# Optimization experiments

Hardware: AMD Instinct MI355X
Metric: run time of the kernel (lower is better)

Reference implementation:

```python
import jax, jax.numpy as jnp
import numpy as np

B, L, D, H = 4, 2048, 1024, 16
DH = D // H

def setup_inputs() -> dict:
    key = jax.random.key(0)
    ks = jax.random.split(key, 9)
    s = 1.0 / np.sqrt(D)
    x = jax.random.normal(ks[0], (B, L, D), dtype=jnp.float32)
    Wq = jax.random.uniform(ks[1], (D, D), jnp.float32, -s, s)
    bq = jax.random.uniform(ks[2], (D,), jnp.float32, -s, s)
    Wk = jax.random.uniform(ks[3], (D, D), jnp.float32, -s, s)
    bk = jax.random.uniform(ks[4], (D,), jnp.float32, -s, s)
    Wv = jax.random.uniform(ks[5], (D, D), jnp.float32, -s, s)
    bv = jax.random.uniform(ks[6], (D,), jnp.float32, -s, s)
    Wo = jax.random.uniform(ks[7], (D, D), jnp.float32, -s, s)
    bo = jax.random.uniform(ks[8], (D,), jnp.float32, -s, s)
    mask = jnp.tril(jnp.ones((L, L), dtype=jnp.int32))[None, None]  # [1,1,L,L] causal
    return {"x": x, "Wq": Wq, "bq": bq, "Wk": Wk, "bk": bk, "Wv": Wv, "bv": bv,
            "Wo": Wo, "bo": bo, "mask": mask}

def reference(x, Wq, bq, Wk, bk, Wv, bv, Wo, bo, mask):
    # projections (torch Linear: x @ W.T + b; here W stored transposed already as [D,D])
    q = (x @ Wq + bq).reshape(B, L, H, DH).transpose(0, 2, 1, 3)  # [B,H,L,Dh]
    k = (x @ Wk + bk).reshape(B, L, H, DH).transpose(0, 2, 1, 3)
    v = (x @ Wv + bv).reshape(B, L, H, DH).transpose(0, 2, 1, 3)
    scores = jnp.einsum('bhqd,bhkd->bhqk', q, k) / jnp.sqrt(jnp.float32(DH))
    scores = jnp.where(mask == 0, -jnp.inf, scores)
    attn = jax.nn.softmax(scores, axis=-1)
    out = jnp.einsum('bhqk,bhkd->bhqd', attn, v)  # [B,H,L,Dh]
    out = out.transpose(0, 2, 1, 3).reshape(B, L, D)
    return out @ Wo + bo
```

## Files before the change

### kernel.cpp

```cpp
#include <hip/hip_runtime.h>
#include <hip/hip_bf16.h>


typedef __bf16 bf16;
typedef __bf16 bf16x4 __attribute__((ext_vector_type(4)));
typedef __bf16 bf16x8 __attribute__((ext_vector_type(8)));
typedef float f32x4 __attribute__((ext_vector_type(4)));

#define DEV static __device__ __forceinline__

constexpr int B = 4, L = 2048, D = 1024, H = 16, DH = 64;
constexpr int BL = B * L;
constexpr int GM = 8192, GK = 1024;
constexpr int BKg = 64;
constexpr int PST = 72;

typedef __attribute__((address_space(1))) const void* gptr1;
typedef __attribute__((address_space(3))) void* lptr3;

DEV void load_lds16(const bf16* g, bf16* l) {
  __builtin_amdgcn_global_load_lds((gptr1)g, (lptr3)l, 16, 0, 0);
}

DEV f32x4 mfma(bf16x8 a, bf16x8 b, f32x4 c) {
  return __builtin_amdgcn_mfma_f32_16x16x32_bf16(a, b, c, 0, 0, 0);
}

DEV float scrub(float v) { return (v == v) ? v : 0.f; }

__global__ void sniff_k(const unsigned short* __restrict__ xr, int* flag) {
  __shared__ int cnt;
  if (threadIdx.x == 0) cnt = 0;
  __syncthreads();
  int local = 0;
  for (int i = threadIdx.x; i < 4096; i += 64) {
    const unsigned short u = xr[2 * i];
    const int e = (u >> 7) & 0xFF;
    if (e >= 0x70 && e <= 0x85) local++;
  }
  atomicAdd(&cnt, local);
  __syncthreads();
  if (threadIdx.x == 0) *flag = (cnt > 2048) ? 1 : 0;
}

__global__ __launch_bounds__(256) void cvt_x_k(const void* __restrict__ src,
                                               bf16* __restrict__ dst,
                                               const int* __restrict__ flag, int n) {
  const bool isbf = (*flag != 0);
  const int stride = gridDim.x * blockDim.x * 8;
  for (int idx = (blockIdx.x * blockDim.x + threadIdx.x) * 8; idx < n; idx += stride) {
    bf16x8 o;
    if (isbf) {
      bf16x8 v = *(const bf16x8*)((const bf16*)src + idx);
      #pragma unroll
      for (int j = 0; j < 8; ++j) o[j] = (bf16)scrub((float)v[j]);
    } else {
      const float* s = (const float*)src + idx;
      #pragma unroll
      for (int j = 0; j < 8; ++j) o[j] = (bf16)scrub(s[j]);
    }
    *(bf16x8*)&dst[idx] = o;
  }
}

__global__ __launch_bounds__(256) void wtrans_cvt4_k(const void* __restrict__ W0,
                                                     const void* __restrict__ W1,
                                                     const void* __restrict__ W2,
                                                     const void* __restrict__ W3,
                                                     bf16* __restrict__ dstBase,
                                                     const int* __restrict__ flag) {
  __shared__ bf16 t[32][33];
  const bool isbf = (*flag != 0);
  const int z = blockIdx.z;
  const void* src = (z == 0) ? W0 : (z == 1) ? W1 : (z == 2) ? W2 : W3;
  bf16* dst = dstBase + (size_t)z * D * D;
  const int bx = blockIdx.x * 32, by = blockIdx.y * 32;
  const int tx = threadIdx.x & 31, ty = threadIdx.x >> 5;
  for (int i = ty; i < 32; i += 8) {
    const size_t off = (size_t)(by + i) * D + bx + tx;
    const float v = isbf ? (float)((const bf16*)src)[off] : ((const float*)src)[off];
    t[i][tx] = (bf16)scrub(v);
  }
  __syncthreads();
  for (int i = ty; i < 32; i += 8)
    dst[(size_t)(bx + i) * D + by + tx] = t[tx][i];
}

__global__ __launch_bounds__(256) void vtrans_k(const bf16* __restrict__ V,
                                                bf16* __restrict__ VT) {
  __shared__ __align__(16) bf16 t[64 * 72];
  const int l0 = blockIdx.x * 64, bh = blockIdx.y;
  const int b = bh >> 4, h = bh & 15;
  const int tid = threadIdx.x;
  #pragma unroll
  for (int i = 0; i < 2; ++i) {
    const int o = tid * 8 + i * 2048;
    const int lrow = o >> 6, dcol = o & 63;
    *(bf16x8*)&t[lrow * 72 + dcol] =
        *(const bf16x8*)&V[(size_t)(b * L + l0 + lrow) * D + h * 64 + dcol];
  }
  __syncthreads();
  const int d = tid >> 2, lg = (tid & 3) * 16;
  bf16x8 o0, o1;
  #pragma unroll
  for (int j = 0; j < 8; ++j) o0[j] = t[(lg + j) * 72 + d];
  #pragma unroll
  for (int j = 0; j < 8; ++j) o1[j] = t[(lg + 8 + j) * 72 + d];
  bf16* dst = VT + ((size_t)bh * DH + d) * L + l0 + lg;
  *(bf16x8*)dst = o0;
  *(bf16x8*)(dst + 8) = o1;
}

__global__ __launch_bounds__(256) void qkv_gemm_k(const bf16* __restrict__ A,
                                                  const bf16* __restrict__ Bt,
                                                  const void* __restrict__ bq,
                                                  const void* __restrict__ bk,
                                                  const void* __restrict__ bv,
                                                  bf16* __restrict__ Q,
                                                  bf16* __restrict__ Kk,
                                                  bf16* __restrict__ V,
                                                  const int* __restrict__ flag) {
  __shared__ __align__(16) bf16 As[128 * BKg];
  __shared__ __align__(16) bf16 Bs[128 * BKg];
  const bool isbf = (*flag != 0);
  const int m0 = blockIdx.x * 128, n0 = blockIdx.y * 128;
  const int buf = n0 >> 10, nloc = n0 & 1023;
  bf16* Cb = (buf == 0) ? Q : (buf == 1) ? Kk : V;
  const void* bias = (buf == 0) ? bq : (buf == 1) ? bk : bv;
  const float scale = (buf == 0) ? 0.18033688011111f : 1.0f;

  const int tid = threadIdx.x, wave = tid >> 6, lane = tid & 63;
  const int wr = wave >> 1, wc = wave & 1;
  const int quad = lane >> 4, l16 = lane & 15;
  const int srow = lane >> 3;
  const int scol = ((lane ^ srow) & 7) * 8;
  const int l7 = l16 & 7;
  const int s0 = ((quad ^ l7) * 8);
  const int s1 = s0 ^ 32;

  f32x4 acc[4][4] = {};

  for (int k0 = 0; k0 < GK; k0 += BKg) {
    for (int c = wave; c < 16; c += 4) {
      load_lds16(A  + (size_t)(m0 + c * 8 + srow) * GK + k0 + scol, &As[c * 512]);
      load_lds16(Bt + (size_t)(n0 + c * 8 + srow) * GK + k0 + scol, &Bs[c * 512]);
    }
    __syncthreads();
    #pragma unroll
    for (int kk = 0; kk < BKg; kk += 32) {
      const int sk = kk ? s1 : s0;
      bf16x8 af[4], bfr[4];
      #pragma unroll
      for (int i = 0; i < 4; ++i)
        af[i] = *(const bf16x8*)&As[(wr * 64 + i * 16 + l16) * BKg + sk];
      #pragma unroll
      for (int i = 0; i < 4; ++i)
        bfr[i] = *(const bf16x8*)&Bs[(wc * 64 + i * 16 + l16) * BKg + sk];
      #pragma unroll
      for (int mi = 0; mi < 4; ++mi)
        #pragma unroll
        for (int ni = 0; ni < 4; ++ni)
          acc[mi][ni] = mfma(af[mi], bfr[ni], acc[mi][ni]);
    }
    __syncthreads();
  }

  #pragma unroll
  for (int ni = 0; ni < 4; ++ni) {
    const int col = nloc + wc * 64 + ni * 16 + l16;
    const float bv2 = isbf ? (float)((const bf16*)bias)[col] : ((const float*)bias)[col];
    #pragma unroll
    for (int mi = 0; mi < 4; ++mi)
      #pragma unroll
      for (int r = 0; r < 4; ++r) {
        const int row = m0 + wr * 64 + mi * 16 + quad * 4 + r;
        Cb[(size_t)row * D + col] = (bf16)((acc[mi][ni][r] + bv2) * scale);
      }
  }
}

__global__ __launch_bounds__(256) void gemm_bt_k(const bf16* __restrict__ A,
                                                 const bf16* __restrict__ Bt,
                                                 const void* __restrict__ bias,
                                                 void* __restrict__ C,
                                                 const int* __restrict__ flag) {
  __shared__ __align__(16) bf16 As[128 * BKg];
  __shared__ __align__(16) bf16 Bs[128 * BKg];
  const bool isbf = (*flag != 0);
  const int m0 = blockIdx.x * 128, n0 = blockIdx.y * 128;
  const int tid = threadIdx.x, wave = tid >> 6, lane = tid & 63;
  const int wr = wave >> 1, wc = wave & 1;
  const int quad = lane >> 4, l16 = lane & 15;
  const int srow = lane >> 3;
  const int scol = ((lane ^ srow) & 7) * 8;
  const int l7 = l16 & 7;
  const int s0 = ((quad ^ l7) * 8);
  const int s1 = s0 ^ 32;

  f32x4 acc[4][4] = {};

  for (int k0 = 0; k0 < GK; k0 += BKg) {
    for (int c = wave; c < 16; c += 4) {
      load_lds16(A  + (size_t)(m0 + c * 8 + srow) * GK + k0 + scol, &As[c * 512]);
      load_lds16(Bt + (size_t)(n0 + c * 8 + srow) * GK + k0 + scol, &Bs[c * 512]);
    }
    __syncthreads();
    #pragma unroll
    for (int kk = 0; kk < BKg; kk += 32) {
      const int sk = kk ? s1 : s0;
      bf16x8 af[4], bfr[4];
      #pragma unroll
      for (int i = 0; i < 4; ++i)
        af[i] = *(const bf16x8*)&As[(wr * 64 + i * 16 + l16) * BKg + sk];
      #pragma unroll
      for (int i = 0; i < 4; ++i)
        bfr[i] = *(const bf16x8*)&Bs[(wc * 64 + i * 16 + l16) * BKg + sk];
      #pragma unroll
      for (int mi = 0; mi < 4; ++mi)
        #pragma unroll
        for (int ni = 0; ni < 4; ++ni)
          acc[mi][ni] = mfma(af[mi], bfr[ni], acc[mi][ni]);
    }
    __syncthreads();
  }

  bf16* Cb = (bf16*)C;
  float* Cf = (float*)C;
  #pragma unroll
  for (int ni = 0; ni < 4; ++ni) {
    const int col = n0 + wc * 64 + ni * 16 + l16;
    const float bv = isbf ? (float)((const bf16*)bias)[col] : ((const float*)bias)[col];
    #pragma unroll
    for (int mi = 0; mi < 4; ++mi)
      #pragma unroll
      for (int r = 0; r < 4; ++r) {
        const int row = m0 + wr * 64 + mi * 16 + quad * 4 + r;
        const float v = acc[mi][ni][r] + bv;
        if (isbf) Cb[(size_t)row * D + col] = (bf16)v;
        else      Cf[(size_t)row * D + col] = v;
      }
  }
}

__global__ __launch_bounds__(256) void attn_k(bf16* QO,
                                              const bf16* __restrict__ K,
                                              const bf16* __restrict__ VT) {
  __shared__ __align__(16) bf16 Ks[64 * DH];
  __shared__ __align__(16) bf16 Vt[DH * 64];
  __shared__ __align__(16) bf16 Ps[4][16 * PST];

  const int bx = blockIdx.x;
  const int qt = (L / 64 - 1) - (bx >> 6);
  const int bh = bx & 63;
  const int b = bh >> 4, h = bh & 15;
  const int tid = threadIdx.x, wave = tid >> 6, lane = tid & 63;
  const int quad = lane >> 4, l16 = lane & 15;
  const int srow = lane >> 3;
  const int scol = ((lane ^ srow) & 7) * 8;
  const int l7 = l16 & 7;
  const int s0 = ((quad ^ l7) * 8);
  const int s1 = s0 ^ 32;

  bf16* Qb = QO + (size_t)b * L * D + h * DH;
  const bf16* Kb = K + (size_t)b * L * D + h * DH;
  const bf16* VTg = VT + (size_t)bh * DH * L;

  const int qrow = qt * 64 + wave * 16 + l16;
  const bf16x8 qf0 = *(const bf16x8*)(Qb + (size_t)qrow * D + quad * 8);
  const bf16x8 qf1 = *(const bf16x8*)(Qb + (size_t)qrow * D + 32 + quad * 8);

  bf16x8 ones;
  #pragma unroll
  for (int j = 0; j < 8; ++j) ones[j] = (bf16)1.0f;

  float m_run = -INFINITY;
  f32x4 o_acc[4] = {};
  f32x4 o_sum = {};

  for (int kt = 0; kt <= qt; ++kt) {
    for (int c = wave; c < 8; c += 4) {
      load_lds16(Kb  + (size_t)(kt * 64 + c * 8 + srow) * D + scol, &Ks[c * 512]);
      load_lds16(VTg + (size_t)(c * 8 + srow) * L + kt * 64 + scol, &Vt[c * 512]);
    }
    __syncthreads();

    f32x4 s[4];
    #pragma unroll
    for (int nb = 0; nb < 4; ++nb) {
      bf16x8 k0 = *(const bf16x8*)&Ks[(nb * 16 + l16) * DH + s0];
      bf16x8 k1 = *(const bf16x8*)&Ks[(nb * 16 + l16) * DH + s1];
      f32x4 a = {};
      a = mfma(k0, qf0, a);
      a = mfma(k1, qf1, a);
      s[nb] = a;
    }

    if (kt == qt) {
      const int qloc = wave * 16 + l16;
      #pragma unroll
      for (int nb = 0; nb < 4; ++nb)
        #pragma unroll
        for (int r = 0; r < 4; ++r)
          if (nb * 16 + quad * 4 + r > qloc) s[nb][r] = -1e30f;
    }

    float mx = -INFINITY;
    #pragma unroll
    for (int nb = 0; nb < 4; ++nb) {
      const float a = fmaxf(fmaxf(s[nb][0], s[nb][1]), fmaxf(s[nb][2], s[nb][3]));
      mx = fmaxf(mx, a);
    }
    mx = fmaxf(mx, __shfl_xor(mx, 16, 64));
    mx = fmaxf(mx, __shfl_xor(mx, 32, 64));

    if (!__all(mx <= m_run + 8.f)) {
      const float mn = fmaxf(m_run, mx);
      const float alpha = __builtin_amdgcn_exp2f(m_run - mn);
      m_run = mn;
      #pragma unroll
      for (int r = 0; r < 4; ++r) {
        const float ar = __shfl(alpha, quad * 4 + r, 64);
        o_sum[r] *= ar;
        #pragma unroll
        for (int db = 0; db < 4; ++db) o_acc[db][r] *= ar;
      }
    }

    bf16* Pw = &Ps[wave][0];
    #pragma unroll
    for (int nb = 0; nb < 4; ++nb) {
      bf16x4 pk;
      #pragma unroll
      for (int r = 0; r < 4; ++r)
        pk[r] = (bf16)__builtin_amdgcn_exp2f(s[nb][r] - m_run);
      *(bf16x4*)&Pw[l16 * PST + nb * 16 + quad * 4] = pk;
    }

    bf16x8 p0 = *(const bf16x8*)&Pw[l16 * PST + quad * 8];
    bf16x8 p1 = *(const bf16x8*)&Pw[l16 * PST + 32 + quad * 8];
    o_sum = mfma(p0, ones, o_sum);
    o_sum = mfma(p1, ones, o_sum);
    #pragma unroll
    for (int db = 0; db < 4; ++db) {
      bf16x8 v0 = *(const bf16x8*)&Vt[(db * 16 + l16) * 64 + s0];
      bf16x8 v1 = *(const bf16x8*)&Vt[(db * 16 + l16) * 64 + s1];
      o_acc[db] = mfma(p0, v0, o_acc[db]);
      o_acc[db] = mfma(p1, v1, o_acc[db]);
    }
    __syncthreads();
  }

  #pragma unroll
  for (int r = 0; r < 4; ++r) {
    const float inv = 1.f / o_sum[r];
    const int row = qt * 64 + wave * 16 + quad * 4 + r;
    #pragma unroll
    for (int db = 0; db < 4; ++db)
      Qb[(size_t)row * D + db * 16 + l16] = (bf16)(o_acc[db][r] * inv);
  }
}

extern "C" void kernel_launch(void* const* d_in, const int* in_sizes, int n_in,
                              void* d_out, int out_size, void* d_ws, size_t ws_size,
                              hipStream_t stream) {
  const void* x  = d_in[0];
  const void* Wq = d_in[1];
  const void* bq = d_in[2];
  const void* Wk = d_in[3];
  const void* bk = d_in[4];
  const void* Wv = d_in[5];
  const void* bv = d_in[6];
  const void* Wo = d_in[7];
  const void* bo = d_in[8];

  int* flag = (int*)d_ws;
  char* p = (char*)d_ws + 4096;
  bf16* xc  = (bf16*)p;                 p += (size_t)BL * D * 2;
  bf16* WqT = (bf16*)p;                 p += (size_t)D * D * 2;
  bf16* WkT = (bf16*)p;                 p += (size_t)D * D * 2;
  bf16* WvT = (bf16*)p;                 p += (size_t)D * D * 2;
  bf16* WoT = (bf16*)p;                 p += (size_t)D * D * 2;
  bf16* Qb  = (bf16*)p;                 p += (size_t)BL * D * 2;
  bf16* Kb  = (bf16*)p;                 p += (size_t)BL * D * 2;
  bf16* Vb  = (bf16*)p;
  bf16* VTb = xc;

  sniff_k<<<1, 64, 0, stream>>>((const unsigned short*)x, flag);

  cvt_x_k<<<1024, 256, 0, stream>>>(x, xc, flag, BL * D);
  wtrans_cvt4_k<<<dim3(32, 32, 4), 256, 0, stream>>>(Wq, Wk, Wv, Wo, WqT, flag);

  qkv_gemm_k<<<dim3(GM / 128, 3072 / 128), 256, 0, stream>>>(
      xc, WqT, bq, bk, bv, Qb, Kb, Vb, flag);

  vtrans_k<<<dim3(L / 64, B * H), 256, 0, stream>>>(Vb, VTb);

  attn_k<<<dim3((L / 64) * B * H), 256, 0, stream>>>(Qb, Kb, VTb);

  gemm_bt_k<<<dim3(GM / 128, D / 128), 256, 0, stream>>>(Qb, WoT, bo, d_out, flag);
}
```

Before: 291.0 us.

## Process two query tiles per attention block with double-buffered K/V loads

The attention kernel now handles 128 query rows per block as two 64-row sub-tiles, so each K/V tile loaded into LDS feeds both sub-tiles, and K/V fragments are read into registers once per tile. K and V^T tiles are double-buffered so the next tile's global-to-LDS load is issued before computing on the current one, overlapping memory with MFMA work. The grid is halved to 1024 blocks, which lowers parallelism and adds register and LDS pressure. It may also make causal load imbalance coarser.

```diff
diff --git a/kernel.cpp b/kernel.cpp
--- a/kernel.cpp
+++ b/kernel.cpp
@@ -245,12 +245,12 @@
 __global__ __launch_bounds__(256) void attn_k(bf16* QO,
                                               const bf16* __restrict__ K,
                                               const bf16* __restrict__ VT) {
-  __shared__ __align__(16) bf16 Ks[64 * DH];
-  __shared__ __align__(16) bf16 Vt[DH * 64];
+  __shared__ __align__(16) bf16 Ks[2][64 * DH];
+  __shared__ __align__(16) bf16 Vt[2][DH * 64];
   __shared__ __align__(16) bf16 Ps[4][16 * PST];
 
   const int bx = blockIdx.x;
-  const int qt = (L / 64 - 1) - (bx >> 6);
+  const int qt = (L / 128 - 1) - (bx >> 6);
   const int bh = bx & 63;
   const int b = bh >> 4, h = bh & 15;
   const int tid = threadIdx.x, wave = tid >> 6, lane = tid & 63;
@@ -265,99 +265,140 @@
   const bf16* Kb = K + (size_t)b * L * D + h * DH;
   const bf16* VTg = VT + (size_t)bh * DH * L;
 
-  const int qrow = qt * 64 + wave * 16 + l16;
-  const bf16x8 qf0 = *(const bf16x8*)(Qb + (size_t)qrow * D + quad * 8);
-  const bf16x8 qf1 = *(const bf16x8*)(Qb + (size_t)qrow * D + 32 + quad * 8);
+  bf16x8 qf[2][2];
+  #pragma unroll
+  for (int sq = 0; sq < 2; ++sq) {
+    const int qrow = qt * 128 + sq * 64 + wave * 16 + l16;
+    qf[sq][0] = *(const bf16x8*)(Qb + (size_t)qrow * D + quad * 8);
+    qf[sq][1] = *(const bf16x8*)(Qb + (size_t)qrow * D + 32 + quad * 8);
+  }
 
   bf16x8 ones;
   #pragma unroll
   for (int j = 0; j < 8; ++j) ones[j] = (bf16)1.0f;
 
-  float m_run = -INFINITY;
-  f32x4 o_acc[4] = {};
-  f32x4 o_sum = {};
-
-  for (int kt = 0; kt <= qt; ++kt) {
-    for (int c = wave; c < 8; c += 4) {
-      load_lds16(Kb  + (size_t)(kt * 64 + c * 8 + srow) * D + scol, &Ks[c * 512]);
-      load_lds16(VTg + (size_t)(c * 8 + srow) * L + kt * 64 + scol, &Vt[c * 512]);
-    }
-    __syncthreads();
-
-    f32x4 s[4];
+  float m_run[2] = {-INFINITY, -INFINITY};
+  f32x4 o_acc[2][4] = {};
+  f32x4 o_sum[2] = {};
+
+  const int nkt = 2 * qt + 2;
+
+  for (int c = wave; c < 8; c += 4) {
+    load_lds16(Kb  + (size_t)(c * 8 + srow) * D + scol, &Ks[0][c * 512]);
+    load_lds16(VTg + (size_t)(c * 8 + srow) * L + scol, &Vt[0][c * 512]);
+  }
+  __syncthreads();
+
+  int cur = 0;
+  for (int kt = 0; kt < nkt; ++kt) {
+    if (kt + 1 < nkt) {
+      const int kn = kt + 1;
+      for (int c = wave; c < 8; c += 4) {
+        load_lds16(Kb  + (size_t)(kn * 64 + c * 8 + srow) * D + scol,
+                   &Ks[cur ^ 1][c * 512]);
+        load_lds16(VTg + (size_t)(c * 8 + srow) * L + kn * 64 + scol,
+                   &Vt[cur ^ 1][c * 512]);
+      }
+    }
+
+    const bf16* Kc = &Ks[cur][0];
+    const bf16* Vc = &Vt[cur][0];
+
+    bf16x8 kf0[4], kf1[4];
     #pragma unroll
     for (int nb = 0; nb < 4; ++nb) {
-      bf16x8 k0 = *(const bf16x8*)&Ks[(nb * 16 + l16) * DH + s0];
-      bf16x8 k1 = *(const bf16x8*)&Ks[(nb * 16 + l16) * DH + s1];
-      f32x4 a = {};
-      a = mfma(k0, qf0, a);
-      a = mfma(k1, qf1, a);
-      s[nb] = a;
-    }
-
-    if (kt == qt) {
-      const int qloc = wave * 16 + l16;
-      #pragma unroll
-      for (int nb = 0; nb < 4; ++nb)
+      kf0[nb] = *(const bf16x8*)&Kc[(nb * 16 + l16) * DH + s0];
+      kf1[nb] = *(const bf16x8*)&Kc[(nb * 16 + l16) * DH + s1];
+    }
+
+    bf16x8 vf0[4], vf1[4];
+    #pragma unroll
+    for (int db = 0; db < 4; ++db) {
+      vf0[db] = *(const bf16x8*)&Vc[(db * 16 + l16) * 64 + s0];
+      vf1[db] = *(const bf16x8*)&Vc[(db * 16 + l16) * 64 + s1];
+    }
+
+    bf16* Pw = &Ps[wave][0];
+
+    #pragma unroll
+    for (int sq = 0; sq < 2; ++sq) {
+      if (sq == 0 && kt == 2 * qt + 1) continue;
+      const bool diag = (kt == 2 * qt + sq);
+
+      f32x4 s[4];
+      #pragma unroll
+      for (int nb = 0; nb < 4; ++nb) {
+        f32x4 a = {};
+        a = mfma(kf0[nb], qf[sq][0], a);
+        a = mfma(kf1[nb], qf[sq][1], a);
+        s[nb] = a;
+      }
+
+      if (diag) {
+        const int qloc = wave * 16 + l16;
+        #pragma unroll
+        for (int nb = 0; nb < 4; ++nb)
+          #pragma unroll
+          for (int r = 0; r < 4; ++r)
+            if (nb * 16 + quad * 4 + r > qloc) s[nb][r] = -1e30f;
+      }
+
+      float mx = -INFINITY;
+      #pragma unroll
+      for (int nb = 0; nb < 4; ++nb) {
+        const float a = fmaxf(fmaxf(s[nb][0], s[nb][1]), fmaxf(s[nb][2], s[nb][3]));
+        mx = fmaxf(mx, a);
+      }
+      mx = fmaxf(mx, __shfl_xor(mx, 16, 64));
+      mx = fmaxf(mx, __shfl_xor(mx, 32, 64));
+
+      if (!__all(mx <= m_run[sq] + 8.f)) {
+        const float mn = fmaxf(m_run[sq], mx);
+        const float alpha = __builtin_amdgcn_exp2f(m_run[sq] - mn);
+        m_run[sq] = mn;
+        #pragma unroll
+        for (int r = 0; r < 4; ++r) {
+          const float ar = __shfl(alpha, quad * 4 + r, 64);
+          o_sum[sq][r] *= ar;
+          #pragma unroll
+          for (int db = 0; db < 4; ++db) o_acc[sq][db][r] *= ar;
+        }
+      }
+
+      #pragma unroll
+      for (int nb = 0; nb < 4; ++nb) {
+        bf16x4 pk;
         #pragma unroll
         for (int r = 0; r < 4; ++r)
-          if (nb * 16 + quad * 4 + r > qloc) s[nb][r] = -1e30f;
-    }
-
-    float mx = -INFINITY;
-    #pragma unroll
-    for (int nb = 0; nb < 4; ++nb) {
-      const float a = fmaxf(fmaxf(s[nb][0], s[nb][1]), fmaxf(s[nb][2], s[nb][3]));
-      mx = fmaxf(mx, a);
-    }
-    mx = fmaxf(mx, __shfl_xor(mx, 16, 64));
-    mx = fmaxf(mx, __shfl_xor(mx, 32, 64));
-
-    if (!__all(mx <= m_run + 8.f)) {
-      const float mn = fmaxf(m_run, mx);
-      const float alpha = __builtin_amdgcn_exp2f(m_run - mn);
-      m_run = mn;
-      #pragma unroll
-      for (int r = 0; r < 4; ++r) {
-        const float ar = __shfl(alpha, quad * 4 + r, 64);
-        o_sum[r] *= ar;
-        #pragma unroll
-        for (int db = 0; db < 4; ++db) o_acc[db][r] *= ar;
-      }
-    }
-
-    bf16* Pw = &Ps[wave][0];
-    #pragma unroll
-    for (int nb = 0; nb < 4; ++nb) {
-      bf16x4 pk;
-      #pragma unroll
-      for (int r = 0; r < 4; ++r)
-        pk[r] = (bf16)__builtin_amdgcn_exp2f(s[nb][r] - m_run);
-      *(bf16x4*)&Pw[l16 * PST + nb * 16 + quad * 4] = pk;
-    }
-
-    bf16x8 p0 = *(const bf16x8*)&Pw[l16 * PST + quad * 8];
-    bf16x8 p1 = *(const bf16x8*)&Pw[l16 * PST + 32 + quad * 8];
-    o_sum = mfma(p0, ones, o_sum);
-    o_sum = mfma(p1, ones, o_sum);
-    #pragma unroll
-    for (int db = 0; db < 4; ++db) {
-      bf16x8 v0 = *(const bf16x8*)&Vt[(db * 16 + l16) * 64 + s0];
-      bf16x8 v1 = *(const bf16x8*)&Vt[(db * 16 + l16) * 64 + s1];
-      o_acc[db] = mfma(p0, v0, o_acc[db]);
-      o_acc[db] = mfma(p1, v1, o_acc[db]);
-    }
+          pk[r] = (bf16)__builtin_amdgcn_exp2f(s[nb][r] - m_run[sq]);
+        *(bf16x4*)&Pw[l16 * PST + nb * 16 + quad * 4] = pk;
+      }
+
+      bf16x8 p0 = *(const bf16x8*)&Pw[l16 * PST + quad * 8];
+      bf16x8 p1 = *(const bf16x8*)&Pw[l16 * PST + 32 + quad * 8];
+      o_sum[sq] = mfma(p0, ones, o_sum[sq]);
+      o_sum[sq] = mfma(p1, ones, o_sum[sq]);
+      #pragma unroll
+      for (int db = 0; db < 4; ++db) {
+        o_acc[sq][db] = mfma(p0, vf0[db], o_acc[sq][db]);
+        o_acc[sq][db] = mfma(p1, vf1[db], o_acc[sq][db]);
+      }
+    }
+
     __syncthreads();
-  }
-
-  #pragma unroll
-  for (int r = 0; r < 4; ++r) {
-    const float inv = 1.f / o_sum[r];
-    const int row = qt * 64 + wave * 16 + quad * 4 + r;
-    #pragma unroll
-    for (int db = 0; db < 4; ++db)
-      Qb[(size_t)row * D + db * 16 + l16] = (bf16)(o_acc[db][r] * inv);
-  }
+    cur ^= 1;
+  }
+
+  #pragma unroll
+  for (int sq = 0; sq < 2; ++sq)
+    #pragma unroll
+    for (int r = 0; r < 4; ++r) {
+      const float inv = 1.f / o_sum[sq][r];
+      const int row = qt * 128 + sq * 64 + wave * 16 + quad * 4 + r;
+      #pragma unroll
+      for (int db = 0; db < 4; ++db)
+        Qb[(size_t)row * D + db * 16 + l16] = (bf16)(o_acc[sq][db][r] * inv);
+    }
 }
 
 extern "C" void kernel_launch(void* const* d_in, const int* in_sizes, int n_in,
@@ -395,7 +436,7 @@
 
   vtrans_k<<<dim3(L / 64, B * H), 256, 0, stream>>>(Vb, VTb);
 
-  attn_k<<<dim3((L / 64) * B * H), 256, 0, stream>>>(Qb, Kb, VTb);
+  attn_k<<<dim3((L / 128) * B * H), 256, 0, stream>>>(Qb, Kb, VTb);
 
   gemm_bt_k<<<dim3(GM / 128, D / 128), 256, 0, stream>>>(Qb, WoT, bo, d_out, flag);
 }
```

Measured after the change: 302.0 us. 3.8% more time.

## Double-buffer K/V tiles and keep P in registers in attention

Applied to the files above, without the earlier changes.

The attention kernel now double-buffers the K and V^T tiles in LDS and prefetches the next tile with async global-to-LDS loads while the current tile is computed. It also builds the P operand straight from the score registers instead of round-tripping through a per-wave LDS buffer. To match that register layout, the V transpose kernel permutes its key columns when writing V^T, so the PV product stays consistent. The aim is to hide global load latency and cut LDS traffic, at the cost of twice the K/V LDS footprint and a layout dependency between the two kernels.

```diff
diff --git a/kernel.cpp b/kernel.cpp
--- a/kernel.cpp
+++ b/kernel.cpp
@@ -13,7 +13,6 @@
 constexpr int BL = B * L;
 constexpr int GM = 8192, GK = 1024;
 constexpr int BKg = 64;
-constexpr int PST = 72;
 
 typedef __attribute__((address_space(1))) const void* gptr1;
 typedef __attribute__((address_space(3))) void* lptr3;
@@ -100,15 +99,18 @@
         *(const bf16x8*)&V[(size_t)(b * L + l0 + lrow) * D + h * 64 + dcol];
   }
   __syncthreads();
-  const int d = tid >> 2, lg = (tid & 3) * 16;
+  const int d = tid >> 2, kc = tid & 3;
+  const int G = kc >> 1, hh = kc & 1;
   bf16x8 o0, o1;
   #pragma unroll
-  for (int j = 0; j < 8; ++j) o0[j] = t[(lg + j) * 72 + d];
-  #pragma unroll
-  for (int j = 0; j < 8; ++j) o1[j] = t[(lg + 8 + j) * 72 + d];
-  bf16* dst = VT + ((size_t)bh * DH + d) * L + l0 + lg;
-  *(bf16x8*)dst = o0;
-  *(bf16x8*)(dst + 8) = o1;
+  for (int j = 0; j < 8; ++j) o0[j] = t[(kc * 16 + j) * 72 + d];
+  #pragma unroll
+  for (int j = 0; j < 8; ++j) o1[j] = t[(kc * 16 + 8 + j) * 72 + d];
+  bf16* dst = VT + ((size_t)bh * DH + d) * L + l0 + G * 32;
+  *(bf16x4*)(dst + hh * 4)      = __builtin_shufflevector(o0, o0, 0, 1, 2, 3);
+  *(bf16x4*)(dst + 8 + hh * 4)  = __builtin_shufflevector(o0, o0, 4, 5, 6, 7);
+  *(bf16x4*)(dst + 16 + hh * 4) = __builtin_shufflevector(o1, o1, 0, 1, 2, 3);
+  *(bf16x4*)(dst + 24 + hh * 4) = __builtin_shufflevector(o1, o1, 4, 5, 6, 7);
 }
 
 __global__ __launch_bounds__(256) void qkv_gemm_k(const bf16* __restrict__ A,
@@ -245,9 +247,8 @@
 __global__ __launch_bounds__(256) void attn_k(bf16* QO,
                                               const bf16* __restrict__ K,
                                               const bf16* __restrict__ VT) {
-  __shared__ __align__(16) bf16 Ks[64 * DH];
-  __shared__ __align__(16) bf16 Vt[DH * 64];
-  __shared__ __align__(16) bf16 Ps[4][16 * PST];
+  __shared__ __align__(16) bf16 Ks[2][64 * 64];
+  __shared__ __align__(16) bf16 Vt[2][64 * 64];
 
   const int bx = blockIdx.x;
   const int qt = (L / 64 - 1) - (bx >> 6);
@@ -277,37 +278,52 @@
   f32x4 o_acc[4] = {};
   f32x4 o_sum = {};
 
-  for (int kt = 0; kt <= qt; ++kt) {
-    for (int c = wave; c < 8; c += 4) {
-      load_lds16(Kb  + (size_t)(kt * 64 + c * 8 + srow) * D + scol, &Ks[c * 512]);
-      load_lds16(VTg + (size_t)(c * 8 + srow) * L + kt * 64 + scol, &Vt[c * 512]);
-    }
-    __syncthreads();
+  const int nkt = qt + 1;
+
+  for (int c = wave; c < 8; c += 4) {
+    load_lds16(Kb  + (size_t)(c * 8 + srow) * D + scol, &Ks[0][c * 512]);
+    load_lds16(VTg + (size_t)(c * 8 + srow) * L + scol, &Vt[0][c * 512]);
+  }
+  __syncthreads();
+
+  int cur = 0;
+  for (int kt = 0; kt < nkt; ++kt) {
+    if (kt + 1 < nkt) {
+      for (int c = wave; c < 8; c += 4) {
+        load_lds16(Kb  + (size_t)((kt + 1) * 64 + c * 8 + srow) * D + scol,
+                   &Ks[cur ^ 1][c * 512]);
+        load_lds16(VTg + (size_t)(c * 8 + srow) * L + (kt + 1) * 64 + scol,
+                   &Vt[cur ^ 1][c * 512]);
+      }
+    }
+
+    const bf16* Kc = &Ks[cur][0];
+    const bf16* Vc = &Vt[cur][0];
 
     f32x4 s[4];
     #pragma unroll
-    for (int nb = 0; nb < 4; ++nb) {
-      bf16x8 k0 = *(const bf16x8*)&Ks[(nb * 16 + l16) * DH + s0];
-      bf16x8 k1 = *(const bf16x8*)&Ks[(nb * 16 + l16) * DH + s1];
+    for (int sub = 0; sub < 4; ++sub) {
+      bf16x8 k0 = *(const bf16x8*)&Kc[(sub * 16 + l16) * 64 + s0];
+      bf16x8 k1 = *(const bf16x8*)&Kc[(sub * 16 + l16) * 64 + s1];
       f32x4 a = {};
       a = mfma(k0, qf0, a);
       a = mfma(k1, qf1, a);
-      s[nb] = a;
+      s[sub] = a;
     }
 
     if (kt == qt) {
       const int qloc = wave * 16 + l16;
       #pragma unroll
-      for (int nb = 0; nb < 4; ++nb)
+      for (int sub = 0; sub < 4; ++sub)
         #pragma unroll
         for (int r = 0; r < 4; ++r)
-          if (nb * 16 + quad * 4 + r > qloc) s[nb][r] = -1e30f;
+          if (sub * 16 + quad * 4 + r > qloc) s[sub][r] = -1e30f;
     }
 
     float mx = -INFINITY;
     #pragma unroll
-    for (int nb = 0; nb < 4; ++nb) {
-      const float a = fmaxf(fmaxf(s[nb][0], s[nb][1]), fmaxf(s[nb][2], s[nb][3]));
+    for (int sub = 0; sub < 4; ++sub) {
+      const float a = fmaxf(fmaxf(s[sub][0], s[sub][1]), fmaxf(s[sub][2], s[sub][3]));
       mx = fmaxf(mx, a);
     }
     mx = fmaxf(mx, __shfl_xor(mx, 16, 64));
@@ -326,28 +342,27 @@
       }
     }
 
-    bf16* Pw = &Ps[wave][0];
-    #pragma unroll
-    for (int nb = 0; nb < 4; ++nb) {
-      bf16x4 pk;
-      #pragma unroll
-      for (int r = 0; r < 4; ++r)
-        pk[r] = (bf16)__builtin_amdgcn_exp2f(s[nb][r] - m_run);
-      *(bf16x4*)&Pw[l16 * PST + nb * 16 + quad * 4] = pk;
-    }
-
-    bf16x8 p0 = *(const bf16x8*)&Pw[l16 * PST + quad * 8];
-    bf16x8 p1 = *(const bf16x8*)&Pw[l16 * PST + 32 + quad * 8];
-    o_sum = mfma(p0, ones, o_sum);
-    o_sum = mfma(p1, ones, o_sum);
+    bf16x8 fr0, fr1;
+    #pragma unroll
+    for (int r = 0; r < 4; ++r) {
+      fr0[r]     = (bf16)__builtin_amdgcn_exp2f(s[0][r] - m_run);
+      fr0[4 + r] = (bf16)__builtin_amdgcn_exp2f(s[1][r] - m_run);
+      fr1[r]     = (bf16)__builtin_amdgcn_exp2f(s[2][r] - m_run);
+      fr1[4 + r] = (bf16)__builtin_amdgcn_exp2f(s[3][r] - m_run);
+    }
+
+    o_sum = mfma(fr0, ones, o_sum);
+    o_sum = mfma(fr1, ones, o_sum);
     #pragma unroll
     for (int db = 0; db < 4; ++db) {
-      bf16x8 v0 = *(const bf16x8*)&Vt[(db * 16 + l16) * 64 + s0];
-      bf16x8 v1 = *(const bf16x8*)&Vt[(db * 16 + l16) * 64 + s1];
-      o_acc[db] = mfma(p0, v0, o_acc[db]);
-      o_acc[db] = mfma(p1, v1, o_acc[db]);
-    }
+      bf16x8 v0 = *(const bf16x8*)&Vc[(db * 16 + l16) * 64 + s0];
+      bf16x8 v1 = *(const bf16x8*)&Vc[(db * 16 + l16) * 64 + s1];
+      o_acc[db] = mfma(fr0, v0, o_acc[db]);
+      o_acc[db] = mfma(fr1, v1, o_acc[db]);
+    }
+
     __syncthreads();
+    cur ^= 1;
   }
 
   #pragma unroll
```

Result: slower. 300.0 us (+3.1%).
